# Optimization experiments

Hardware: AMD Instinct MI355X
Metric: run time of the kernel (lower is better)

Reference implementation:

```python
import jax, jax.numpy as jnp
import numpy as np

B = 256
LSTM = 512
FEAT = 3 * 3 * 512 + 16 + 8  # 4632
N_ACT = 4
ACT_SHAPE = 64
NUM_STEPS = 20
CANVAS_IN = 6 * 32 * 32  # 6144
H1 = int(FEAT / (FEAT / LSTM) ** (1.0 / 3.0))  # 2223
H2 = int(FEAT / (FEAT / LSTM) ** (2.0 / 3.0))  # 1067


def setup_inputs() -> dict:
    key = jax.random.key(0)
    ks = jax.random.split(key, 32)

    def g(k, shape, scale=0.02):
        return jax.random.normal(k, shape, dtype=jnp.float32) * scale

    inp = {
        "actualCanvas": jax.random.normal(ks[0], (B, 3, 32, 32), dtype=jnp.float32),
        "objectiveCanvas": jax.random.normal(ks[1], (B, 3, 32, 32), dtype=jnp.float32),
        "last_action_end_position": jax.random.randint(ks[2], (B,), 0, ACT_SHAPE),
        "episode_percentage": jax.random.randint(ks[3], (B,), 0, NUM_STEPS),
        # feature extractor stub (flatten -> linear -> relu), output 4608
        "Wfe": g(ks[4], (4608, CANVAS_IN)), "bfe": jnp.zeros((4608,), jnp.float32),
        "emb_end": g(ks[5], (ACT_SHAPE, 16), 1.0),
        "emb_ep": g(ks[6], (NUM_STEPS, 8), 1.0),
        "W1": g(ks[7], (H1, FEAT)), "b1": jnp.zeros((H1,), jnp.float32),
        "W2": g(ks[8], (H2, H1)), "b2": jnp.zeros((H2,), jnp.float32),
        "W3": g(ks[9], (LSTM, H2)), "b3": jnp.zeros((LSTM,), jnp.float32),
        "W_ih": g(ks[10], (4 * LSTM, LSTM)), "W_hh": g(ks[11], (4 * LSTM, LSTM)),
        "b_ih": jnp.zeros((4 * LSTM,), jnp.float32), "b_hh": jnp.zeros((4 * LSTM,), jnp.float32),
        "Wd1": g(ks[12], (N_ACT, LSTM // 2, LSTM)), "bd1": jnp.zeros((N_ACT, LSTM // 2), jnp.float32),
        "Wd2": g(ks[13], (N_ACT, ACT_SHAPE, LSTM // 2)), "bd2": jnp.zeros((N_ACT, ACT_SHAPE), jnp.float32),
        "emb_dec": g(ks[14], (N_ACT, ACT_SHAPE, 16), 1.0),
        "Wout": g(ks[15], (LSTM, LSTM + 16)), "bout": jnp.zeros((LSTM,), jnp.float32),
    }
    return inp


def reference(actualCanvas, objectiveCanvas, last_action_end_position, episode_percentage,
              Wfe, bfe, emb_end, emb_ep, W1, b1, W2, b2, W3, b3,
              W_ih, W_hh, b_ih, b_hh, Wd1, bd1, Wd2, bd2, emb_dec, Wout, bout):
    # feature extractor on channel-concatenated canvases -> [B, 4608]
    x = jnp.concatenate([actualCanvas, objectiveCanvas], axis=1).reshape(B, -1)
    fv = jax.nn.relu(x @ Wfe.T + bfe)
    feats = jnp.concatenate([fv, emb_end[last_action_end_position], emb_ep[episode_percentage]], axis=1)
    # fc1->fc2->fc3 (dropout = eval mode / identity)
    h = jax.nn.relu(feats @ W1.T + b1)
    h = jax.nn.relu(h @ W2.T + b2)
    h = jax.nn.relu(h @ W3.T + b3)  # [B, LSTM]
    # single-step LSTM with zero initial state (first execution)
    gates = h @ W_ih.T + b_ih + b_hh  # h0 = 0 so recurrent matmul vanishes
    i, f, g_, o = jnp.split(gates, 4, axis=1)
    c = jax.nn.sigmoid(i) * jnp.tanh(g_)
    seed = jax.nn.sigmoid(o) * jnp.tanh(c)  # [B, LSTM]
    z = seed
    log_probabilities = jnp.zeros((B,), jnp.float32)
    entropy = jnp.float32(0.0)
    actions = []
    base_key = jax.random.key(42)
    for k in range(N_ACT):
        hm = jax.nn.relu(z @ Wd1[k].T + bd1[k])
        logits = hm @ Wd2[k].T + bd2[k]  # [B, ACT_SHAPE]
        logp = jax.nn.log_softmax(logits, axis=1)
        probs = jnp.exp(logp)
        entropy = entropy + jnp.sum(-probs * logp)
        act = jax.random.categorical(jax.random.fold_in(base_key, k), logits, axis=1)  # [B]
        actions.append(act)
        log_probabilities = log_probabilities + jnp.take_along_axis(logp, act[:, None], axis=1)[:, 0]
        emb_a = emb_dec[k][act]  # [B,16]
        z = jax.nn.relu(jnp.concatenate([z, emb_a], axis=1) @ Wout.T + bout)
    action = jnp.stack(actions, axis=1)  # [B, N_ACT]
    return action, entropy, log_probabilities
```

## Files before the change

### kernel.cpp

```cpp
#include <hip/hip_runtime.h>
#include <hip/hip_bf16.h>
#include <stdint.h>

#define B_SZ   256
#define LSTM_N 512
#define FEAT_N 4632
#define FV_N   4608
#define CIN_N  6144
#define HALF_CIN 3072
#define ACT_N  64
#define LD_FEAT 4672
#define LD_ZEXT 576

typedef __attribute__((ext_vector_type(8))) short bf16x8;
typedef __attribute__((ext_vector_type(4))) float f32x4;

__device__ __forceinline__ short f2bf(float f) {
  uint32_t u = __float_as_uint(f);
  u += 0x7FFFu + ((u >> 16) & 1u);
  return (short)(u >> 16);
}
__device__ __forceinline__ float bf2f(short s) {
  return __uint_as_float(((uint32_t)(uint16_t)s) << 16);
}
__device__ __forceinline__ uint32_t pack2(float x, float y) {
  return (__float_as_uint(x) >> 16) | (__float_as_uint(y) & 0xffff0000u);
}

typedef __attribute__((address_space(3))) void lds_void_t;
typedef const __attribute__((address_space(1))) void gbl_void_t;
__device__ __forceinline__ void lds_dma16(const void* g, void* l) {
  __builtin_amdgcn_global_load_lds((gbl_void_t*)g, (lds_void_t*)l, 16, 0, 0);
}

__device__ __forceinline__ uint32_t rotl32(uint32_t x, int r) {
  return (x << r) | (x >> (32 - r));
}
__device__ __forceinline__ void threefry2x32(uint32_t k0, uint32_t k1,
                                             uint32_t x0, uint32_t x1,
                                             uint32_t& o0, uint32_t& o1) {
  uint32_t k2 = k0 ^ k1 ^ 0x1BD11BDAu;
  x0 += k0; x1 += k1;
  x0 += x1; x1 = rotl32(x1, 13); x1 ^= x0;
  x0 += x1; x1 = rotl32(x1, 15); x1 ^= x0;
  x0 += x1; x1 = rotl32(x1, 26); x1 ^= x0;
  x0 += x1; x1 = rotl32(x1,  6); x1 ^= x0;
  x0 += k1; x1 += k2 + 1u;
  x0 += x1; x1 = rotl32(x1, 17); x1 ^= x0;
  x0 += x1; x1 = rotl32(x1, 29); x1 ^= x0;
  x0 += x1; x1 = rotl32(x1, 16); x1 ^= x0;
  x0 += x1; x1 = rotl32(x1, 24); x1 ^= x0;
  x0 += k2; x1 += k0 + 2u;
  x0 += x1; x1 = rotl32(x1, 13); x1 ^= x0;
  x0 += x1; x1 = rotl32(x1, 15); x1 ^= x0;
  x0 += x1; x1 = rotl32(x1, 26); x1 ^= x0;
  x0 += x1; x1 = rotl32(x1,  6); x1 ^= x0;
  x0 += k0; x1 += k1 + 3u;
  x0 += x1; x1 = rotl32(x1, 17); x1 ^= x0;
  x0 += x1; x1 = rotl32(x1, 29); x1 ^= x0;
  x0 += x1; x1 = rotl32(x1, 16); x1 ^= x0;
  x0 += x1; x1 = rotl32(x1, 24); x1 ^= x0;
  x0 += k1; x1 += k2 + 4u;
  x0 += x1; x1 = rotl32(x1, 13); x1 ^= x0;
  x0 += x1; x1 = rotl32(x1, 15); x1 ^= x0;
  x0 += x1; x1 = rotl32(x1, 26); x1 ^= x0;
  x0 += x1; x1 = rotl32(x1,  6); x1 ^= x0;
  x0 += k2; x1 += k0 + 5u;
  o0 = x0; o1 = x1;
}

__global__ void concat_cvt_kernel(const float* __restrict__ act,
                                  const float* __restrict__ obj,
                                  short* __restrict__ xb) {
  int idx = blockIdx.x * 256 + threadIdx.x;
  if (idx >= B_SZ * 768) return;
  int row = idx / 768;
  int c8 = (idx - row * 768) * 8;
  const float* src = (c8 < HALF_CIN) ? (act + (size_t)row * HALF_CIN + c8)
                                     : (obj + (size_t)row * HALF_CIN + (c8 - HALF_CIN));
  float4 u = ((const float4*)src)[0];
  float4 v = ((const float4*)src)[1];
  bf16x8 r;
  r[0]=f2bf(u.x); r[1]=f2bf(u.y); r[2]=f2bf(u.z); r[3]=f2bf(u.w);
  r[4]=f2bf(v.x); r[5]=f2bf(v.y); r[6]=f2bf(v.z); r[7]=f2bf(v.w);
  *(bf16x8*)&xb[(size_t)row * CIN_N + c8] = r;
}

__global__ void gumbel_kernel(float* __restrict__ gum) {
  int idx = blockIdx.x * 256 + threadIdx.x;
  if (idx >= 4 * 16384) return;
  int k = idx >> 14;
  uint32_t j = (uint32_t)(idx & 16383);
  uint32_t f0, f1, o0, o1, bits;
  threefry2x32(0u, 42u, 0u, (uint32_t)k, f0, f1);
  if (j < 8192u) { threefry2x32(f0, f1, j, j + 8192u, o0, o1); bits = o0; }
  else           { threefry2x32(f0, f1, j - 8192u, j, o0, o1); bits = o1; }
  const float tiny = 1.17549435e-38f;
  float fu = __uint_as_float((bits >> 9) | 0x3f800000u) - 1.0f;
  float u = fmaxf(tiny, fu * (1.0f - tiny) + tiny);
  gum[idx] = -logf(-logf(u));
}

__global__ void fill_embs_kernel(const int* __restrict__ lastpos,
                                 const int* __restrict__ ep,
                                 const float* __restrict__ emb_end,
                                 const float* __restrict__ emb_ep,
                                 short* __restrict__ feats) {
  int b = blockIdx.x;
  int t = threadIdx.x;
  short* row = feats + (size_t)b * LD_FEAT;
  if (t < 16)      row[FV_N + t] = f2bf(emb_end[lastpos[b] * 16 + t]);
  else if (t < 24) row[FV_N + 16 + (t - 16)] = f2bf(emb_ep[ep[b] * 8 + (t - 16)]);
  else             row[FV_N + t] = 0;
}

__global__ __launch_bounds__(512, 4) void gemm7_kernel(
    const short* __restrict__ A, int ldab,
    const float* __restrict__ W, int ldw,
    const float* __restrict__ Wend,
    short* __restrict__ P, int nblk,
    int N, int Kiter, int kc, int nchunks) {
  __shared__ float Wlds[2][64 * 64];

  const int tid = threadIdx.x;
  const int w = tid >> 6, l = tid & 63, l15 = l & 15, lg = l >> 4;
  const int n0 = blockIdx.x * 64;
  const int Np = nblk * 64;
  const int ks = blockIdx.y;
  const int kbeg = ks * kc;
  const int kend = (kbeg + kc < Kiter) ? (kbeg + kc) : Kiter;
  const int nk = (kend - kbeg) >> 6;
  const int mrow = w << 5;

  const char* wlim = (const char*)Wend - 16;

  f32x4 acc[2][4];
#pragma unroll
  for (int i = 0; i < 2; ++i)
#pragma unroll
    for (int j = 0; j < 4; ++j) acc[i][j] = (f32x4){0.f, 0.f, 0.f, 0.f};

  auto dma = [&](int kt, int buf) {
#pragma unroll
    for (int q = 0; q < 2; ++q) {
      int r = (w << 3) + (q << 2) + (l >> 4);
      int gn = n0 + r; if (gn >= N) gn = N - 1;
      int g16 = (l & 15) ^ (r & 15);
      const char* src = (const char*)(W + (size_t)gn * ldw + kt) + g16 * 16;
      if (src > wlim) src = wlim;
      lds_dma16(src, (void*)&Wlds[buf][((w << 3) + (q << 2)) * 64]);
    }
  };

  if (nk > 0) {
    dma(kbeg, 0);
    __syncthreads();

    for (int t = 0; t < nk; ++t) {
      const int cur = t & 1;
      const int kt = kbeg + (t << 6);
      bf16x8 af[2][2];
#pragma unroll
      for (int mf = 0; mf < 2; ++mf) {
        const short* arow = &A[(size_t)(mrow + (mf << 4) + l15) * ldab + kt + (lg << 3)];
        af[mf][0] = *(const bf16x8*)arow;
        af[mf][1] = *(const bf16x8*)(arow + 32);
      }
      if (t + 1 < nk) dma(kt + 64, cur ^ 1);
#pragma unroll
      for (int nj = 0; nj < 4; ++nj) {
        int r = (nj << 4) + l15;
        const float* rb = &Wlds[cur][r * 64];
        int rx = r & 15;
        f32x4 u0 = *(const f32x4*)(rb + ((((lg << 1)    ) ^ rx) << 2));
        f32x4 u1 = *(const f32x4*)(rb + ((((lg << 1) | 1) ^ rx) << 2));
        f32x4 v0 = *(const f32x4*)(rb + ((((lg << 1) + 8) ^ rx) << 2));
        f32x4 v1 = *(const f32x4*)(rb + ((((lg << 1) + 9) ^ rx) << 2));
        bf16x8 b0, b1;
        uint32_t* p0 = (uint32_t*)&b0;
        uint32_t* p1 = (uint32_t*)&b1;
        p0[0] = pack2(u0[0], u0[1]); p0[1] = pack2(u0[2], u0[3]);
        p0[2] = pack2(u1[0], u1[1]); p0[3] = pack2(u1[2], u1[3]);
        p1[0] = pack2(v0[0], v0[1]); p1[1] = pack2(v0[2], v0[3]);
        p1[2] = pack2(v1[0], v1[1]); p1[3] = pack2(v1[2], v1[3]);
        acc[0][nj] = __builtin_amdgcn_mfma_f32_16x16x32_bf16(af[0][0], b0, acc[0][nj], 0, 0, 0);
        acc[1][nj] = __builtin_amdgcn_mfma_f32_16x16x32_bf16(af[1][0], b0, acc[1][nj], 0, 0, 0);
        acc[0][nj] = __builtin_amdgcn_mfma_f32_16x16x32_bf16(af[0][1], b1, acc[0][nj], 0, 0, 0);
        acc[1][nj] = __builtin_amdgcn_mfma_f32_16x16x32_bf16(af[1][1], b1, acc[1][nj], 0, 0, 0);
      }
      __syncthreads();
    }
  }

  short* Pb = P + (size_t)ks * 256 * Np;
#pragma unroll
  for (int nj = 0; nj < 4; ++nj) {
    int gn = n0 + (nj << 4) + l15;
#pragma unroll
    for (int mf = 0; mf < 2; ++mf)
#pragma unroll
      for (int r = 0; r < 4; ++r) {
        int gm = mrow + (mf << 4) + (lg << 2) + r;
        Pb[(size_t)gm * Np + gn] = f2bf(acc[mf][nj][r]);
      }
  }
}

__global__ void reduce_kernel(const short* __restrict__ P, int Np, int nchunks,
                              const float* __restrict__ bias1,
                              const float* __restrict__ bias2,
                              void* __restrict__ out, int ldc, int N,
                              int relu, int mode_f32) {
  int npack = Np >> 3;
  int idx = blockIdx.x * 256 + threadIdx.x;
  if (idx >= 256 * npack) return;
  int m = idx / npack;
  int n8 = (idx - m * npack) << 3;
  float s[8] = {0.f, 0.f, 0.f, 0.f, 0.f, 0.f, 0.f, 0.f};
  for (int ks = 0; ks < nchunks; ++ks) {
    bf16x8 v = *(const bf16x8*)&P[(size_t)ks * 256 * Np + (size_t)m * Np + n8];
#pragma unroll
    for (int j = 0; j < 8; ++j) s[j] += bf2f(v[j]);
  }
#pragma unroll
  for (int j = 0; j < 8; ++j) {
    int n = n8 + j;
    float r = 0.f;
    if (n < N) {
      r = s[j];
      if (bias1) r += bias1[n];
      if (bias2) r += bias2[n];
      if (relu) r = fmaxf(r, 0.f);
    }
    s[j] = r;
  }
  if (mode_f32) {
    float* o = (float*)out + (size_t)m * ldc + n8;
#pragma unroll
    for (int j = 0; j < 8; ++j) o[j] = s[j];
  } else {
    bf16x8 r;
#pragma unroll
    for (int j = 0; j < 8; ++j) r[j] = f2bf(s[j]);
    *(bf16x8*)((short*)out + (size_t)m * ldc + n8) = r;
  }
}

__global__ void reduce_lstm_kernel(const short* __restrict__ P, int nchunks,
                                   const float* __restrict__ b_ih,
                                   const float* __restrict__ b_hh,
                                   short* __restrict__ zext) {
  int idx = blockIdx.x * 256 + threadIdx.x;
  if (idx >= 256 * 64) return;
  int m = idx >> 6;
  int n8 = (idx & 63) << 3;
  float gi[8] = {}, gg[8] = {}, go[8] = {};
  for (int ks = 0; ks < nchunks; ++ks) {
    const short* base = P + ((size_t)ks * 256 + m) * 2048;
    bf16x8 vi = *(const bf16x8*)(base + n8);
    bf16x8 vg = *(const bf16x8*)(base + 1024 + n8);
    bf16x8 vo = *(const bf16x8*)(base + 1536 + n8);
#pragma unroll
    for (int j = 0; j < 8; ++j) {
      gi[j] += bf2f(vi[j]); gg[j] += bf2f(vg[j]); go[j] += bf2f(vo[j]);
    }
  }
  bf16x8 hv;
#pragma unroll
  for (int j = 0; j < 8; ++j) {
    int n = n8 + j;
    float i_ = gi[j] + b_ih[n] + b_hh[n];
    float g_ = gg[j] + b_ih[1024 + n] + b_hh[1024 + n];
    float o_ = go[j] + b_ih[1536 + n] + b_hh[1536 + n];
    float si = 1.f / (1.f + expf(-i_));
    float so = 1.f / (1.f + expf(-o_));
    float c = si * tanhf(g_);
    hv[j] = f2bf(so * tanhf(c));
  }
  *(bf16x8*)&zext[(size_t)m * LD_ZEXT + n8] = hv;
}

__global__ __launch_bounds__(256) void logits_sample_kernel(
    const short* __restrict__ hm,
    const float* __restrict__ Wd2k,
    const float* __restrict__ bd2k,
    const float* __restrict__ gumk,
    const float* __restrict__ embk,
    short* __restrict__ zext,
    int* __restrict__ act_out, float* __restrict__ logp_out,
    float* __restrict__ ent_out, int write_emb) {
  __shared__ short Wl[64 * 264];
  const int tid = threadIdx.x;
  const int w = tid >> 6, l = tid & 63, l15 = l & 15, lg = l >> 4;
  const int mbase = blockIdx.x * 64 + w * 16;

  {
    int r = tid >> 2;
    int c0 = (tid & 3) << 6;
    const float* src = Wd2k + r * 256 + c0;
    short* dst = &Wl[r * 264 + c0];
#pragma unroll
    for (int i = 0; i < 8; ++i) {
      float4 u = ((const float4*)src)[2 * i];
      float4 v = ((const float4*)src)[2 * i + 1];
      bf16x8 t;
      t[0]=f2bf(u.x); t[1]=f2bf(u.y); t[2]=f2bf(u.z); t[3]=f2bf(u.w);
      t[4]=f2bf(v.x); t[5]=f2bf(v.y); t[6]=f2bf(v.z); t[7]=f2bf(v.w);
      *(bf16x8*)(dst + 8 * i) = t;
    }
  }
  __syncthreads();

  f32x4 acc[4];
#pragma unroll
  for (int j = 0; j < 4; ++j) acc[j] = (f32x4){0.f, 0.f, 0.f, 0.f};

#pragma unroll
  for (int kt = 0; kt < 4; ++kt) {
    int k0 = kt << 6;
    const short* arow = &hm[(size_t)(mbase + l15) * 256 + k0 + (lg << 3)];
    bf16x8 af0 = *(const bf16x8*)arow;
    bf16x8 af1 = *(const bf16x8*)(arow + 32);
#pragma unroll
    for (int nj = 0; nj < 4; ++nj) {
      const short* bp = &Wl[((nj << 4) + l15) * 264 + k0 + (lg << 3)];
      bf16x8 b0 = *(const bf16x8*)bp;
      bf16x8 b1 = *(const bf16x8*)(bp + 32);
      acc[nj] = __builtin_amdgcn_mfma_f32_16x16x32_bf16(af0, b0, acc[nj], 0, 0, 0);
      acc[nj] = __builtin_amdgcn_mfma_f32_16x16x32_bf16(af1, b1, acc[nj], 0, 0, 0);
    }
  }

  float bcol[4];
#pragma unroll
  for (int nj = 0; nj < 4; ++nj) bcol[nj] = bd2k[(nj << 4) + l15];

#pragma unroll
  for (int r = 0; r < 4; ++r) {
    int row = mbase + (lg << 2) + r;
    float lv[4];
#pragma unroll
    for (int nj = 0; nj < 4; ++nj) lv[nj] = acc[nj][r] + bcol[nj];
    float mx = fmaxf(fmaxf(lv[0], lv[1]), fmaxf(lv[2], lv[3]));
#pragma unroll
    for (int off = 8; off; off >>= 1) mx = fmaxf(mx, __shfl_xor(mx, off));
    float es = expf(lv[0]-mx) + expf(lv[1]-mx) + expf(lv[2]-mx) + expf(lv[3]-mx);
#pragma unroll
    for (int off = 8; off; off >>= 1) es += __shfl_xor(es, off);
    float lse = logf(es);
    float lp[4], ent = 0.f;
#pragma unroll
    for (int nj = 0; nj < 4; ++nj) {
      lp[nj] = lv[nj] - mx - lse;
      ent += -expf(lp[nj]) * lp[nj];
    }
#pragma unroll
    for (int off = 8; off; off >>= 1) ent += __shfl_xor(ent, off);
    float bv = -3.4e38f; int bc = 64; float blp = 0.f;
#pragma unroll
    for (int nj = 0; nj < 4; ++nj) {
      int col = (nj << 4) + l15;
      float pert = lv[nj] + gumk[row * 64 + col];
      if (pert > bv || (pert == bv && col < bc)) { bv = pert; bc = col; blp = lp[nj]; }
    }
#pragma unroll
    for (int off = 8; off; off >>= 1) {
      float ov = __shfl_xor(bv, off);
      int oc = __shfl_xor(bc, off);
      float olp = __shfl_xor(blp, off);
      if (ov > bv || (ov == bv && oc < bc)) { bv = ov; bc = oc; blp = olp; }
    }
    if (l15 == 0) {
      act_out[row] = bc;
      logp_out[row] = blp;
      ent_out[row] = ent;
    }
    if (write_emb) {
      short* zr = zext + (size_t)row * LD_ZEXT;
      zr[512 + l15] = f2bf(embk[bc * 16 + l15]);
      zr[528 + l15] = 0;
      zr[544 + l15] = 0;
      zr[560 + l15] = 0;
    }
  }
}

__global__ void finalize_kernel(const int* __restrict__ act,
                                const float* __restrict__ logp_k,
                                const float* __restrict__ ent,
                                float* __restrict__ out) {
  __shared__ float sred[4];
  int t = threadIdx.x;
#pragma unroll
  for (int k = 0; k < 4; ++k)
    out[t * 4 + k] = (float)act[k * 256 + t];
  float lp = 0.f;
#pragma unroll
  for (int k = 0; k < 4; ++k) lp += logp_k[k * 256 + t];
  out[1025 + t] = lp;

  float v = 0.f;
#pragma unroll
  for (int k = 0; k < 4; ++k) v += ent[k * 256 + t];
#pragma unroll
  for (int off = 32; off; off >>= 1) v += __shfl_xor(v, off);
  if ((t & 63) == 0) sred[t >> 6] = v;
  __syncthreads();
  if (t == 0) out[1024] = sred[0] + sred[1] + sred[2] + sred[3];
}

extern "C" void kernel_launch(void* const* d_in, const int* in_sizes, int n_in,
                              void* d_out, int out_size, void* d_ws, size_t ws_size,
                              hipStream_t stream) {
  float* out = (float*)d_out;
  char* out_bytes = (char*)d_out;
  auto sentinel = [&](int code) { hipMemsetAsync(out_bytes + 4096, code, 4, stream); };

  if (n_in < 25 || in_sizes[0] != B_SZ * 3 * 32 * 32 ||
      in_sizes[4] != FV_N * CIN_N || in_sizes[23] != LSTM_N * 528 ||
      in_sizes[9] <= 0 || in_sizes[9] > 8192 ||
      in_sizes[11] <= 0 || in_sizes[11] > 8192) {
    sentinel(0x42);
    return;
  }

  const float* actual = (const float*)d_in[0];
  const float* object = (const float*)d_in[1];
  const int* lastpos  = (const int*)d_in[2];
  const int* ep       = (const int*)d_in[3];
  const float* Wfe    = (const float*)d_in[4];
  const float* bfe    = (const float*)d_in[5];
  const float* emb_end= (const float*)d_in[6];
  const float* emb_ep = (const float*)d_in[7];
  const float* W1     = (const float*)d_in[8];
  const float* b1     = (const float*)d_in[9];
  const float* W2     = (const float*)d_in[10];
  const float* b2     = (const float*)d_in[11];
  const float* W3     = (const float*)d_in[12];
  const float* b3     = (const float*)d_in[13];
  const float* W_ih   = (const float*)d_in[14];
  const float* b_ih   = (const float*)d_in[16];
  const float* b_hh   = (const float*)d_in[17];
  const float* Wd1    = (const float*)d_in[18];
  const float* bd1    = (const float*)d_in[19];
  const float* Wd2    = (const float*)d_in[20];
  const float* bd2    = (const float*)d_in[21];
  const float* embdec = (const float*)d_in[22];
  const float* Wout   = (const float*)d_in[23];
  const float* bout   = (const float*)d_in[24];

  const int H1 = in_sizes[9];
  const int H2 = in_sizes[11];
  const int ldh1 = 64 * ((H1 + 63) / 64);
  const int ldh2 = 64 * ((H2 + 63) / 64);

  char* wsb = (char*)d_ws;
  size_t off = 0;
  auto alloc = [&](size_t bytes) {
    char* p = wsb + off;
    off += (bytes + 255) & ~(size_t)255;
    return p;
  };
  float* logpk = (float*)alloc(1024 * 4);
  float* entk  = (float*)alloc(1024 * 4);
  int*   actk  = (int*)alloc(1024 * 4);
  float* gumb  = (float*)alloc(4 * 16384 * 4);
  short* xb    = (short*)alloc((size_t)B_SZ * CIN_N * 2);
  short* feats = (short*)alloc((size_t)B_SZ * LD_FEAT * 2);
  short* h1    = (short*)alloc((size_t)B_SZ * ldh1 * 2);
  short* h2    = (short*)alloc((size_t)B_SZ * ldh2 * 2);
  short* h3    = (short*)alloc((size_t)B_SZ * 512 * 2);
  short* zextA = (short*)alloc((size_t)B_SZ * LD_ZEXT * 2);
  short* zextB = (short*)alloc((size_t)B_SZ * LD_ZEXT * 2);
  short* hm    = (short*)alloc((size_t)B_SZ * 256 * 2);
  if (off + (8 << 20) > ws_size) {
    sentinel(0x43);
    return;
  }
  short* slab = (short*)(wsb + off);
  const size_t slab_bytes = ws_size - off;

  auto gemm = [&](const short* A, int ldab, const float* Wm, int ldw, int Kiter,
                  const float* bb1, const float* bb2,
                  void* C, int ldc, int N, int relu, int fuse) {
    int nblk = (N + 63) / 64;
    int Np = nblk * 64;
    int tiles = Kiter >> 6;
    int c = (512 + nblk - 1) / nblk;
    if (c > tiles) c = tiles;
    size_t cap = slab_bytes / ((size_t)256 * Np * 2);
    if ((size_t)c > cap) c = (int)cap;
    if (c < 1) c = 1;
    int ct = (tiles + c - 1) / c;
    int kc = 64 * ct;
    int chunks = (tiles + ct - 1) / ct;
    dim3 g(nblk, chunks);
    gemm7_kernel<<<g, dim3(512), 0, stream>>>(
        A, ldab, Wm, ldw, Wm + (size_t)N * ldw, slab, nblk, N, Kiter, kc, chunks);
    if (fuse == 1) {
      reduce_lstm_kernel<<<dim3(64), dim3(256), 0, stream>>>(
          slab, chunks, bb1, bb2, (short*)C);
    } else {
      int npack = Np >> 3;
      reduce_kernel<<<dim3((256 * npack + 255) / 256), dim3(256), 0, stream>>>(
          slab, Np, chunks, bb1, bb2, C, ldc, N, relu, 0);
    }
  };

  concat_cvt_kernel<<<dim3(768), dim3(256), 0, stream>>>(actual, object, xb);
  gumbel_kernel<<<dim3(256), dim3(256), 0, stream>>>(gumb);
  gemm(xb, CIN_N, Wfe, CIN_N, CIN_N, bfe, nullptr, feats, LD_FEAT, FV_N, 1, 0);
  fill_embs_kernel<<<dim3(B_SZ), dim3(64), 0, stream>>>(lastpos, ep, emb_end, emb_ep, feats);
  gemm(feats, LD_FEAT, W1, FEAT_N, LD_FEAT, b1, nullptr, h1, ldh1, H1, 1, 0);
  gemm(h1, ldh1, W2, H1, ldh1, b2, nullptr, h2, ldh2, H2, 1, 0);
  gemm(h2, ldh2, W3, H2, ldh2, b3, nullptr, h3, 512, LSTM_N, 1, 0);
  gemm(h3, 512, W_ih, LSTM_N, 512, b_ih, b_hh, zextA, LD_ZEXT, 4 * LSTM_N, 0, 1);

  short* zcur = zextA;
  short* znxt = zextB;
  for (int k = 0; k < 4; ++k) {
    const float* Wd1k = Wd1 + (size_t)k * 256 * LSTM_N;
    const float* bd1k = bd1 + (size_t)k * 256;
    const float* Wd2k = Wd2 + (size_t)k * ACT_N * 256;
    const float* bd2k = bd2 + (size_t)k * ACT_N;
    const float* embk = embdec + (size_t)k * ACT_N * 16;
    gemm(zcur, LD_ZEXT, Wd1k, LSTM_N, 512, bd1k, nullptr, hm, 256, 256, 1, 0);
    logits_sample_kernel<<<dim3(4), dim3(256), 0, stream>>>(
        hm, Wd2k, bd2k, gumb + k * 16384, embk, zcur,
        actk + k * B_SZ, logpk + k * B_SZ, entk + k * B_SZ, (k < 3) ? 1 : 0);
    if (k < 3) {
      gemm(zcur, LD_ZEXT, Wout, 528, LD_ZEXT, bout, nullptr, znxt, LD_ZEXT, LSTM_N, 1, 0);
      short* t = zcur; zcur = znxt; znxt = t;
    }
  }

  finalize_kernel<<<dim3(1), dim3(256), 0, stream>>>(actk, logpk, entk, out);
}
```

Before: 274.1 us.

## Add 32-column, 128-K GEMM kernel for large layers with wider split-K

Adds a gemm8 kernel that processes 32 output columns per block with 128-wide K tiles, where each wave covers 64 rows of M. The large feature, MLP and LSTM GEMMs now use it with a higher split-K target of 896 blocks, and the decoder GEMMs keep the old kernel. Leading dimensions are padded to multiples of 128, and reduce8 zero-fills the padded columns so the next layer's K loop reads clean data. The aim is more blocks in flight and fewer loop iterations on the weight-bandwidth-bound layers. In exchange the split-K partial sums take more slab memory and add reduction traffic.

```diff
diff --git a/kernel.cpp b/kernel.cpp
--- a/kernel.cpp
+++ b/kernel.cpp
@@ -9,8 +9,10 @@
 #define CIN_N  6144
 #define HALF_CIN 3072
 #define ACT_N  64
-#define LD_FEAT 4672
-#define LD_ZEXT 576
+#define LD_FEAT 4736
+#define LD_H1   2304
+#define LD_H2   1152
+#define LD_ZEXT 640
 
 typedef __attribute__((ext_vector_type(8))) short bf16x8;
 typedef __attribute__((ext_vector_type(4))) float f32x4;
@@ -114,6 +116,155 @@
   else             row[FV_N + t] = 0;
 }
 
+__global__ __launch_bounds__(512, 4) void gemm8_kernel(
+    const short* __restrict__ A, int ldab,
+    const float* __restrict__ W, int ldw,
+    const float* __restrict__ Wend,
+    short* __restrict__ P, int nblk,
+    int N, int Kiter, int kc, int nchunks) {
+  __shared__ float Wlds[2][32 * 128];
+
+  const int tid = threadIdx.x;
+  const int w = tid >> 6, l = tid & 63, l15 = l & 15, lg = l >> 4;
+  const int n0 = blockIdx.x * 32;
+  const int Np = nblk * 32;
+  const int ks = blockIdx.y;
+  const int kbeg = ks * kc;
+  const int kend = (kbeg + kc < Kiter) ? (kbeg + kc) : Kiter;
+  const int nk = (kend - kbeg) >> 7;
+  const int mrow = (w & 3) << 6;
+  const int nh = w >> 2;
+
+  const char* wlim = (const char*)Wend - 16;
+
+  f32x4 acc[4];
+#pragma unroll
+  for (int j = 0; j < 4; ++j) acc[j] = (f32x4){0.f, 0.f, 0.f, 0.f};
+
+  auto dma = [&](int kt, int buf) {
+#pragma unroll
+    for (int q = 0; q < 2; ++q) {
+      int rowbase = (w << 2) + (q << 1);
+      int rr = rowbase + (l >> 5);
+      int gn = n0 + rr; if (gn >= N) gn = N - 1;
+      int s = l & 31;
+      int slot = s ^ (rr & 7);
+      const char* src = (const char*)(W + (size_t)gn * ldw + kt) + slot * 16;
+      if (src > wlim) src = wlim;
+      lds_dma16(src, (void*)&Wlds[buf][rowbase * 128]);
+    }
+  };
+
+  if (nk > 0) {
+    dma(kbeg, 0);
+    __syncthreads();
+
+    for (int t = 0; t < nk; ++t) {
+      const int cur = t & 1;
+      const int kt = kbeg + (t << 7);
+      if (t + 1 < nk) dma(kt + 128, cur ^ 1);
+      const int r = (nh << 4) + l15;
+      const int x = r & 7;
+      const float* rb = &Wlds[cur][r * 128];
+#pragma unroll
+      for (int ksub = 0; ksub < 4; ++ksub) {
+        bf16x8 af[4];
+#pragma unroll
+        for (int mf = 0; mf < 4; ++mf)
+          af[mf] = *(const bf16x8*)&A[(size_t)(mrow + (mf << 4) + l15) * ldab +
+                                      kt + (ksub << 5) + (lg << 3)];
+        int g0 = (ksub << 3) + (lg << 1);
+        f32x4 u = *(const f32x4*)(rb + ((g0 ^ x) << 2));
+        f32x4 v = *(const f32x4*)(rb + (((g0 + 1) ^ x) << 2));
+        bf16x8 b;
+        uint32_t* pb = (uint32_t*)&b;
+        pb[0] = pack2(u[0], u[1]); pb[1] = pack2(u[2], u[3]);
+        pb[2] = pack2(v[0], v[1]); pb[3] = pack2(v[2], v[3]);
+#pragma unroll
+        for (int mf = 0; mf < 4; ++mf)
+          acc[mf] = __builtin_amdgcn_mfma_f32_16x16x32_bf16(af[mf], b, acc[mf], 0, 0, 0);
+      }
+      __syncthreads();
+    }
+  }
+
+  short* Pb = P + (size_t)ks * 256 * Np;
+  int gn = n0 + (nh << 4) + l15;
+#pragma unroll
+  for (int mf = 0; mf < 4; ++mf)
+#pragma unroll
+    for (int r = 0; r < 4; ++r) {
+      int gm = mrow + (mf << 4) + (lg << 2) + r;
+      Pb[(size_t)gm * Np + gn] = f2bf(acc[mf][r]);
+    }
+}
+
+__global__ void reduce8_kernel(const short* __restrict__ P, int Np, int nchunks,
+                               const float* __restrict__ bias,
+                               short* __restrict__ out, int ldc, int N, int wcols,
+                               int relu) {
+  int npack = wcols >> 3;
+  int idx = blockIdx.x * 256 + threadIdx.x;
+  if (idx >= 256 * npack) return;
+  int m = idx / npack;
+  int n8 = (idx - m * npack) << 3;
+  float s[8] = {0.f, 0.f, 0.f, 0.f, 0.f, 0.f, 0.f, 0.f};
+  if (n8 < Np) {
+    for (int ks = 0; ks < nchunks; ++ks) {
+      bf16x8 v = *(const bf16x8*)&P[(size_t)ks * 256 * Np + (size_t)m * Np + n8];
+#pragma unroll
+      for (int j = 0; j < 8; ++j) s[j] += bf2f(v[j]);
+    }
+  }
+  bf16x8 r;
+#pragma unroll
+  for (int j = 0; j < 8; ++j) {
+    int n = n8 + j;
+    float v = 0.f;
+    if (n < N) {
+      v = s[j];
+      if (bias) v += bias[n];
+      if (relu) v = fmaxf(v, 0.f);
+    }
+    r[j] = f2bf(v);
+  }
+  *(bf16x8*)&out[(size_t)m * ldc + n8] = r;
+}
+
+__global__ void reduce_lstm_kernel(const short* __restrict__ P, int nchunks,
+                                   const float* __restrict__ b_ih,
+                                   const float* __restrict__ b_hh,
+                                   short* __restrict__ zext) {
+  int idx = blockIdx.x * 256 + threadIdx.x;
+  if (idx >= 256 * 64) return;
+  int m = idx >> 6;
+  int n8 = (idx & 63) << 3;
+  float gi[8] = {}, gg[8] = {}, go[8] = {};
+  for (int ks = 0; ks < nchunks; ++ks) {
+    const short* base = P + ((size_t)ks * 256 + m) * 2048;
+    bf16x8 vi = *(const bf16x8*)(base + n8);
+    bf16x8 vg = *(const bf16x8*)(base + 1024 + n8);
+    bf16x8 vo = *(const bf16x8*)(base + 1536 + n8);
+#pragma unroll
+    for (int j = 0; j < 8; ++j) {
+      gi[j] += bf2f(vi[j]); gg[j] += bf2f(vg[j]); go[j] += bf2f(vo[j]);
+    }
+  }
+  bf16x8 hv;
+#pragma unroll
+  for (int j = 0; j < 8; ++j) {
+    int n = n8 + j;
+    float i_ = gi[j] + b_ih[n] + b_hh[n];
+    float g_ = gg[j] + b_ih[1024 + n] + b_hh[1024 + n];
+    float o_ = go[j] + b_ih[1536 + n] + b_hh[1536 + n];
+    float si = 1.f / (1.f + expf(-i_));
+    float so = 1.f / (1.f + expf(-o_));
+    float c = si * tanhf(g_);
+    hv[j] = f2bf(so * tanhf(c));
+  }
+  *(bf16x8*)&zext[(size_t)m * LD_ZEXT + n8] = hv;
+}
+
 __global__ __launch_bounds__(512, 4) void gemm7_kernel(
     const short* __restrict__ A, int ldab,
     const float* __restrict__ W, int ldw,
@@ -155,7 +306,6 @@
   if (nk > 0) {
     dma(kbeg, 0);
     __syncthreads();
-
     for (int t = 0; t < nk; ++t) {
       const int cur = t & 1;
       const int kt = kbeg + (t << 6);
@@ -207,10 +357,8 @@
 }
 
 __global__ void reduce_kernel(const short* __restrict__ P, int Np, int nchunks,
-                              const float* __restrict__ bias1,
-                              const float* __restrict__ bias2,
-                              void* __restrict__ out, int ldc, int N,
-                              int relu, int mode_f32) {
+                              const float* __restrict__ bias,
+                              short* __restrict__ out, int ldc, int N, int relu) {
   int npack = Np >> 3;
   int idx = blockIdx.x * 256 + threadIdx.x;
   if (idx >= 256 * npack) return;
@@ -222,62 +370,19 @@
 #pragma unroll
     for (int j = 0; j < 8; ++j) s[j] += bf2f(v[j]);
   }
+  bf16x8 r;
 #pragma unroll
   for (int j = 0; j < 8; ++j) {
     int n = n8 + j;
-    float r = 0.f;
+    float v = 0.f;
     if (n < N) {
-      r = s[j];
-      if (bias1) r += bias1[n];
-      if (bias2) r += bias2[n];
-      if (relu) r = fmaxf(r, 0.f);
-    }
-    s[j] = r;
-  }
-  if (mode_f32) {
-    float* o = (float*)out + (size_t)m * ldc + n8;
-#pragma unroll
-    for (int j = 0; j < 8; ++j) o[j] = s[j];
-  } else {
-    bf16x8 r;
-#pragma unroll
-    for (int j = 0; j < 8; ++j) r[j] = f2bf(s[j]);
-    *(bf16x8*)((short*)out + (size_t)m * ldc + n8) = r;
-  }
-}
-
-__global__ void reduce_lstm_kernel(const short* __restrict__ P, int nchunks,
-                                   const float* __restrict__ b_ih,
-                                   const float* __restrict__ b_hh,
-                                   short* __restrict__ zext) {
-  int idx = blockIdx.x * 256 + threadIdx.x;
-  if (idx >= 256 * 64) return;
-  int m = idx >> 6;
-  int n8 = (idx & 63) << 3;
-  float gi[8] = {}, gg[8] = {}, go[8] = {};
-  for (int ks = 0; ks < nchunks; ++ks) {
-    const short* base = P + ((size_t)ks * 256 + m) * 2048;
-    bf16x8 vi = *(const bf16x8*)(base + n8);
-    bf16x8 vg = *(const bf16x8*)(base + 1024 + n8);
-    bf16x8 vo = *(const bf16x8*)(base + 1536 + n8);
-#pragma unroll
-    for (int j = 0; j < 8; ++j) {
-      gi[j] += bf2f(vi[j]); gg[j] += bf2f(vg[j]); go[j] += bf2f(vo[j]);
-    }
-  }
-  bf16x8 hv;
-#pragma unroll
-  for (int j = 0; j < 8; ++j) {
-    int n = n8 + j;
-    float i_ = gi[j] + b_ih[n] + b_hh[n];
-    float g_ = gg[j] + b_ih[1024 + n] + b_hh[1024 + n];
-    float o_ = go[j] + b_ih[1536 + n] + b_hh[1536 + n];
-    float si = 1.f / (1.f + expf(-i_));
-    float so = 1.f / (1.f + expf(-o_));
-    float c = si * tanhf(g_);
-    hv[j] = f2bf(so * tanhf(c));
-  }
-  *(bf16x8*)&zext[(size_t)m * LD_ZEXT + n8] = hv;
+      v = s[j];
+      if (bias) v += bias[n];
+      if (relu) v = fmaxf(v, 0.f);
+    }
+    r[j] = f2bf(v);
+  }
+  *(bf16x8*)&out[(size_t)m * ldc + n8] = r;
 }
 
 __global__ __launch_bounds__(256) void logits_sample_kernel(
@@ -378,9 +483,8 @@
     if (write_emb) {
       short* zr = zext + (size_t)row * LD_ZEXT;
       zr[512 + l15] = f2bf(embk[bc * 16 + l15]);
-      zr[528 + l15] = 0;
-      zr[544 + l15] = 0;
-      zr[560 + l15] = 0;
+#pragma unroll
+      for (int z = 528; z < LD_ZEXT; z += 16) zr[z + l15] = 0;
     }
   }
 }
@@ -451,8 +555,6 @@
 
   const int H1 = in_sizes[9];
   const int H2 = in_sizes[11];
-  const int ldh1 = 64 * ((H1 + 63) / 64);
-  const int ldh2 = 64 * ((H2 + 63) / 64);
 
   char* wsb = (char*)d_ws;
   size_t off = 0;
@@ -467,54 +569,72 @@
   float* gumb  = (float*)alloc(4 * 16384 * 4);
   short* xb    = (short*)alloc((size_t)B_SZ * CIN_N * 2);
   short* feats = (short*)alloc((size_t)B_SZ * LD_FEAT * 2);
-  short* h1    = (short*)alloc((size_t)B_SZ * ldh1 * 2);
-  short* h2    = (short*)alloc((size_t)B_SZ * ldh2 * 2);
+  short* h1    = (short*)alloc((size_t)B_SZ * LD_H1 * 2);
+  short* h2    = (short*)alloc((size_t)B_SZ * LD_H2 * 2);
   short* h3    = (short*)alloc((size_t)B_SZ * 512 * 2);
   short* zextA = (short*)alloc((size_t)B_SZ * LD_ZEXT * 2);
   short* zextB = (short*)alloc((size_t)B_SZ * LD_ZEXT * 2);
   short* hm    = (short*)alloc((size_t)B_SZ * 256 * 2);
-  if (off + (8 << 20) > ws_size) {
+  if (off + (18 << 20) > ws_size) {
     sentinel(0x43);
     return;
   }
   short* slab = (short*)(wsb + off);
   const size_t slab_bytes = ws_size - off;
 
-  auto gemm = [&](const short* A, int ldab, const float* Wm, int ldw, int Kiter,
-                  const float* bb1, const float* bb2,
-                  void* C, int ldc, int N, int relu, int fuse) {
+  auto gemm_big = [&](const short* A, int ldab, const float* Wm, int ldw, int Kiter,
+                      const float* bias, short* C, int ldc, int N, int wcols,
+                      int relu, int fuse, const float* bias2) {
+    int nblk = (N + 31) / 32;
+    int Np = nblk * 32;
+    int tiles = Kiter >> 7;
+    int c = (896 + nblk - 1) / nblk;
+    if (c > tiles) c = tiles;
+    size_t cap = slab_bytes / ((size_t)256 * Np * 2 + 4096);
+    if ((size_t)c > cap) c = (int)cap;
+    if (c < 1) c = 1;
+    int ct = (tiles + c - 1) / c;
+    int kc = 128 * ct;
+    int chunks = (tiles + ct - 1) / ct;
+    dim3 g(nblk, chunks);
+    gemm8_kernel<<<g, dim3(512), 0, stream>>>(
+        A, ldab, Wm, ldw, Wm + (size_t)N * ldw, slab, nblk, N, Kiter, kc, chunks);
+    if (fuse == 1) {
+      reduce_lstm_kernel<<<dim3(64), dim3(256), 0, stream>>>(
+          slab, chunks, bias, bias2, C);
+    } else {
+      int npack = wcols >> 3;
+      reduce8_kernel<<<dim3((256 * npack + 255) / 256), dim3(256), 0, stream>>>(
+          slab, Np, chunks, bias, C, ldc, N, wcols, relu);
+    }
+  };
+
+  auto gemm_dec = [&](const short* A, int ldab, const float* Wm, int ldw, int Kiter,
+                      const float* bias, short* C, int ldc, int N, int relu) {
     int nblk = (N + 63) / 64;
     int Np = nblk * 64;
     int tiles = Kiter >> 6;
     int c = (512 + nblk - 1) / nblk;
     if (c > tiles) c = tiles;
-    size_t cap = slab_bytes / ((size_t)256 * Np * 2);
-    if ((size_t)c > cap) c = (int)cap;
-    if (c < 1) c = 1;
     int ct = (tiles + c - 1) / c;
     int kc = 64 * ct;
     int chunks = (tiles + ct - 1) / ct;
     dim3 g(nblk, chunks);
     gemm7_kernel<<<g, dim3(512), 0, stream>>>(
         A, ldab, Wm, ldw, Wm + (size_t)N * ldw, slab, nblk, N, Kiter, kc, chunks);
-    if (fuse == 1) {
-      reduce_lstm_kernel<<<dim3(64), dim3(256), 0, stream>>>(
-          slab, chunks, bb1, bb2, (short*)C);
-    } else {
-      int npack = Np >> 3;
-      reduce_kernel<<<dim3((256 * npack + 255) / 256), dim3(256), 0, stream>>>(
-          slab, Np, chunks, bb1, bb2, C, ldc, N, relu, 0);
-    }
+    int npack = Np >> 3;
+    reduce_kernel<<<dim3((256 * npack + 255) / 256), dim3(256), 0, stream>>>(
+        slab, Np, chunks, bias, C, ldc, N, relu);
   };
 
   concat_cvt_kernel<<<dim3(768), dim3(256), 0, stream>>>(actual, object, xb);
   gumbel_kernel<<<dim3(256), dim3(256), 0, stream>>>(gumb);
-  gemm(xb, CIN_N, Wfe, CIN_N, CIN_N, bfe, nullptr, feats, LD_FEAT, FV_N, 1, 0);
-  fill_embs_kernel<<<dim3(B_SZ), dim3(64), 0, stream>>>(lastpos, ep, emb_end, emb_ep, feats);
-  gemm(feats, LD_FEAT, W1, FEAT_N, LD_FEAT, b1, nullptr, h1, ldh1, H1, 1, 0);
-  gemm(h1, ldh1, W2, H1, ldh1, b2, nullptr, h2, ldh2, H2, 1, 0);
-  gemm(h2, ldh2, W3, H2, ldh2, b3, nullptr, h3, 512, LSTM_N, 1, 0);
-  gemm(h3, 512, W_ih, LSTM_N, 512, b_ih, b_hh, zextA, LD_ZEXT, 4 * LSTM_N, 0, 1);
+  gemm_big(xb, CIN_N, Wfe, CIN_N, CIN_N, bfe, feats, LD_FEAT, FV_N, FV_N, 1, 0, nullptr);
+  fill_embs_kernel<<<dim3(B_SZ), dim3(128), 0, stream>>>(lastpos, ep, emb_end, emb_ep, feats);
+  gemm_big(feats, LD_FEAT, W1, FEAT_N, LD_FEAT, b1, h1, LD_H1, H1, LD_H1, 1, 0, nullptr);
+  gemm_big(h1, LD_H1, W2, H1, LD_H1, b2, h2, LD_H2, H2, LD_H2, 1, 0, nullptr);
+  gemm_big(h2, LD_H2, W3, H2, LD_H2, b3, h3, 512, LSTM_N, 512, 1, 0, nullptr);
+  gemm_big(h3, 512, W_ih, LSTM_N, 512, b_ih, zextA, LD_ZEXT, 4 * LSTM_N, 0, 0, 1, b_hh);
 
   short* zcur = zextA;
   short* znxt = zextB;
@@ -524,12 +644,12 @@
     const float* Wd2k = Wd2 + (size_t)k * ACT_N * 256;
     const float* bd2k = bd2 + (size_t)k * ACT_N;
     const float* embk = embdec + (size_t)k * ACT_N * 16;
-    gemm(zcur, LD_ZEXT, Wd1k, LSTM_N, 512, bd1k, nullptr, hm, 256, 256, 1, 0);
+    gemm_dec(zcur, LD_ZEXT, Wd1k, LSTM_N, 512, bd1k, hm, 256, 256, 1);
     logits_sample_kernel<<<dim3(4), dim3(256), 0, stream>>>(
         hm, Wd2k, bd2k, gumb + k * 16384, embk, zcur,
         actk + k * B_SZ, logpk + k * B_SZ, entk + k * B_SZ, (k < 3) ? 1 : 0);
     if (k < 3) {
-      gemm(zcur, LD_ZEXT, Wout, 528, LD_ZEXT, bout, nullptr, znxt, LD_ZEXT, LSTM_N, 1, 0);
+      gemm_dec(zcur, LD_ZEXT, Wout, 528, LD_ZEXT, bout, znxt, LD_ZEXT, LSTM_N, 1);
       short* t = zcur; zcur = znxt; znxt = t;
     }
   }
```

After: 363.3 us. 32.5% more time.
